# Kernel tuning notes

Measured on AMD Instinct MI355X. Metric: run time of the kernel, lower is better.

Reference implementation:

```python
import jax, jax.numpy as jnp
import numpy as np

COMMITMENT_COST = 0.25


def setup_inputs() -> dict:
    key = jax.random.key(0)
    k1, k2 = jax.random.split(key)
    cnt_emb = jax.random.normal(k1, (64, 2048, 80), dtype=jnp.float32)
    embed_weight = jax.random.normal(k2, (1024, 80), dtype=jnp.float32)  # nn.Embedding(n_embed, n_mel).weight
    return {"cnt_emb": cnt_emb, "embed_weight": embed_weight}


def reference(cnt_emb, embed_weight):
    # embed: detached, transposed [n_mel, n_embed], column-normalized (only for distance computation)
    embed = jax.lax.stop_gradient(embed_weight).T  # [80, 1024]
    embed = embed / jnp.linalg.norm(embed, axis=0, keepdims=True)

    flatten = jax.lax.stop_gradient(cnt_emb.reshape(-1, cnt_emb.shape[-1]))  # [N, 80]
    dist = (
        jnp.sum(flatten * flatten, axis=1, keepdims=True)
        - 2.0 * (flatten @ embed)
        + jnp.sum(embed * embed, axis=0, keepdims=True)
    )  # [N, n_embed]
    embed_ind = jnp.argmax(-dist, axis=1).reshape(cnt_emb.shape[:-1])  # [B, T]

    # gather from the UNnormalized embedding table (as nn.Embedding lookup)
    quantized = embed_weight[embed_ind]  # [B, T, 80]

    e_latent_loss = jnp.mean((jax.lax.stop_gradient(quantized) - cnt_emb) ** 2)
    q_latent_loss = jnp.mean((quantized - jax.lax.stop_gradient(cnt_emb)) ** 2)
    loss = q_latent_loss + COMMITMENT_COST * e_latent_loss

    # straight-through estimator
    quantized = cnt_emb + jax.lax.stop_gradient(quantized - cnt_emb)
    return quantized, loss
```

## Files before the change

kernel.cpp:

```cpp
#include <hip/hip_runtime.h>

#define D   80
#define NE  1024
#define CAP 32
#define MARGIN 0.5f

#define OFF_ACC  0
#define OFF_EN   64
#define OFF_EC   327744
#define OFF_ENBT 331840
#define OFF_BIDX 495680
#define OFF_CNT  1019968
#define OFF_LIST 1544256
#define WS_NEED  9932864

typedef __attribute__((ext_vector_type(8))) short  bf16x8;
typedef __attribute__((ext_vector_type(4))) float  f32x4;

static __device__ __forceinline__ short f2bf(float f) {
    unsigned u = __float_as_uint(f);
    return (short)((u + 0x7fffu + ((u >> 16) & 1u)) >> 16);
}

static __device__ __forceinline__ bf16x8 cvt8(const float* p) {
    float4 f0 = *(const float4*)p;
    float4 f1 = *(const float4*)(p + 4);
    bf16x8 a;
    a[0] = f2bf(f0.x); a[1] = f2bf(f0.y); a[2] = f2bf(f0.z); a[3] = f2bf(f0.w);
    a[4] = f2bf(f1.x); a[5] = f2bf(f1.y); a[6] = f2bf(f1.z); a[7] = f2bf(f1.w);
    return a;
}

static __device__ __forceinline__ void gload_lds16(const void* g, void* l) {
    __builtin_amdgcn_global_load_lds(
        (const __attribute__((address_space(1))) unsigned int*)g,
        (__attribute__((address_space(3))) unsigned int*)l, 16, 0, 0);
}

__global__ __launch_bounds__(256) void vq_prep(const float* __restrict__ w,
                                               float* __restrict__ en,
                                               float* __restrict__ ec,
                                               char* __restrict__ enbT) {
    int j = blockIdx.x * blockDim.x + threadIdx.x;
    if (j >= NE) return;
    const float* wj = w + j * D;
    float s = __fmul_rn(wj[0], wj[0]);
    for (int k = 1; k < D; ++k) s = __fadd_rn(s, __fmul_rn(wj[k], wj[k]));
    float norm = __fsqrt_rn(s);
    float* ej = en + j * D;
    float c = 0.f;
    for (int k = 0; k < D; ++k) {
        float v = __fdiv_rn(wj[k], norm);
        ej[k] = v;
        float sq = __fmul_rn(v, v);
        c = (k == 0) ? sq : __fadd_rn(c, sq);
    }
    ec[j] = c;
    for (int cc = 0; cc < 10; ++cc) {
        bf16x8 b;
#pragma unroll
        for (int e = 0; e < 8; ++e)
            b[e] = f2bf(__fmul_rn(-2.0f, ej[cc * 8 + e]));
        *(bf16x8*)(enbT + cc * 16384 + j * 16) = b;
    }
}

__global__ __launch_bounds__(256)
__attribute__((amdgpu_waves_per_eu(4, 4)))
void vq_mfma(
        const float* __restrict__ x,
        const char* __restrict__ enbT,
        int* __restrict__ cnt,
        unsigned short* __restrict__ list,
        int n) {
    __shared__ __align__(16) char lds[40960];

    const int tid  = threadIdx.x;
    const int lane = tid & 63;
    const int wv   = tid >> 6;
    const int row0 = blockIdx.x * 128 + wv * 32;
    const int l15  = lane & 15;
    const int lg   = lane >> 4;

    bf16x8 A0[2], A1[2], A2[2];
#pragma unroll
    for (int rt = 0; rt < 2; ++rt) {
        const float* xr = x + (size_t)(row0 + rt * 16 + l15) * D;
        A0[rt] = cvt8(xr + lg * 8);
        A1[rt] = cvt8(xr + 32 + lg * 8);
        if (lg < 2) A2[rt] = cvt8(xr + 64 + lg * 8);
        else { bf16x8 z = {}; A2[rt] = z; }
    }

    const int sl = wv * 1024 + lane * 16;

    float vmin[2][4];
#pragma unroll
    for (int rt = 0; rt < 2; ++rt)
#pragma unroll
        for (int r = 0; r < 4; ++r) vmin[rt][r] = 3.4e38f;

    for (int s = 0; s < 4; ++s) {
        __syncthreads();
#pragma unroll
        for (int c = 0; c < 10; ++c)
            gload_lds16(enbT + c * 16384 + s * 4096 + sl, lds + c * 4096 + sl);
        __syncthreads();

        for (int e16 = 0; e16 < 16; ++e16) {
            const char* base = lds + (e16 * 16 + l15) * 16;
            bf16x8 B0 = *(const bf16x8*)(base + lg * 4096);
            bf16x8 B1 = *(const bf16x8*)(base + (4 + lg) * 4096);
            bf16x8 B2 = *(const bf16x8*)(base + (8 + (lg & 1)) * 4096);
#pragma unroll
            for (int rt = 0; rt < 2; ++rt) {
                f32x4 c = {0.f, 0.f, 0.f, 0.f};
                c = __builtin_amdgcn_mfma_f32_16x16x32_bf16(A0[rt], B0, c, 0, 0, 0);
                c = __builtin_amdgcn_mfma_f32_16x16x32_bf16(A1[rt], B1, c, 0, 0, 0);
                c = __builtin_amdgcn_mfma_f32_16x16x32_bf16(A2[rt], B2, c, 0, 0, 0);
#pragma unroll
                for (int r = 0; r < 4; ++r) vmin[rt][r] = fminf(vmin[rt][r], c[r]);
            }
        }
    }

    float thr[2][4];
#pragma unroll
    for (int rt = 0; rt < 2; ++rt)
#pragma unroll
        for (int r = 0; r < 4; ++r) {
            float v = vmin[rt][r];
#pragma unroll
            for (int m = 1; m < 16; m <<= 1) v = fminf(v, __shfl_xor(v, m));
            thr[rt][r] = v + MARGIN;
        }

    for (int s = 0; s < 4; ++s) {
        __syncthreads();
#pragma unroll
        for (int c = 0; c < 10; ++c)
            gload_lds16(enbT + c * 16384 + s * 4096 + sl, lds + c * 4096 + sl);
        __syncthreads();

        for (int e16 = 0; e16 < 16; ++e16) {
            const char* base = lds + (e16 * 16 + l15) * 16;
            bf16x8 B0 = *(const bf16x8*)(base + lg * 4096);
            bf16x8 B1 = *(const bf16x8*)(base + (4 + lg) * 4096);
            bf16x8 B2 = *(const bf16x8*)(base + (8 + (lg & 1)) * 4096);
            int jj = s * 256 + e16 * 16 + l15;
#pragma unroll
            for (int rt = 0; rt < 2; ++rt) {
                f32x4 c = {0.f, 0.f, 0.f, 0.f};
                c = __builtin_amdgcn_mfma_f32_16x16x32_bf16(A0[rt], B0, c, 0, 0, 0);
                c = __builtin_amdgcn_mfma_f32_16x16x32_bf16(A1[rt], B1, c, 0, 0, 0);
                c = __builtin_amdgcn_mfma_f32_16x16x32_bf16(A2[rt], B2, c, 0, 0, 0);
                bool h0 = c[0] <= thr[rt][0], h1 = c[1] <= thr[rt][1];
                bool h2 = c[2] <= thr[rt][2], h3 = c[3] <= thr[rt][3];
                if (__any(h0 | h1 | h2 | h3)) {
#pragma unroll
                    for (int r = 0; r < 4; ++r) {
                        bool h = (r == 0) ? h0 : (r == 1) ? h1 : (r == 2) ? h2 : h3;
                        if (h) {
                            int row = row0 + rt * 16 + lg * 4 + r;
                            int o = atomicAdd(cnt + row, 1);
                            if (o < CAP)
                                list[(size_t)row * CAP + o] = (unsigned short)jj;
                        }
                    }
                }
            }
        }
    }
}

__global__ __launch_bounds__(256)
__attribute__((amdgpu_waves_per_eu(1, 2)))
void vq_exact(const float* __restrict__ x,
              const float* __restrict__ en,
              const float* __restrict__ ec,
              const int* __restrict__ cnt,
              const unsigned short* __restrict__ list,
              int* __restrict__ bidx, int n) {
    int row = blockIdx.x * 256 + threadIdx.x;
    if (row >= n) return;
    float X[D];
    const float4* x4 = (const float4*)(x + (size_t)row * D);
#pragma unroll
    for (int i = 0; i < D / 4; ++i) {
        float4 v = x4[i];
        X[4 * i + 0] = v.x; X[4 * i + 1] = v.y;
        X[4 * i + 2] = v.z; X[4 * i + 3] = v.w;
    }
    float pr[8];
#pragma unroll
    for (int t = 0; t < 8; ++t) pr[t] = __fmul_rn(X[t], X[t]);
#pragma unroll
    for (int base = 8; base < D; base += 8)
#pragma unroll
        for (int t = 0; t < 8; ++t)
            pr[t] = __fadd_rn(pr[t], __fmul_rn(X[base + t], X[base + t]));
    float A = __fadd_rn(
        __fadd_rn(__fadd_rn(pr[0], pr[1]), __fadd_rn(pr[2], pr[3])),
        __fadd_rn(__fadd_rn(pr[4], pr[5]), __fadd_rn(pr[6], pr[7])));

    float best = 3.4e38f;
    int bi = -1;
    int c = cnt[row];
    if (c > 0 && c <= CAP) {
        for (int i = 0; i < c; ++i) {
            int j = list[(size_t)row * CAP + i];
            const float* ej = en + j * D;
            float d = 0.f;
#pragma unroll
            for (int k = 0; k < D; ++k) d = __builtin_fmaf(X[k], ej[k], d);
            float s = __fadd_rn(__fsub_rn(A, __fmul_rn(2.0f, d)), ec[j]);
            if (s < best || (s == best && j < bi)) { best = s; bi = j; }
        }
    } else {
        for (int j = 0; j < NE; ++j) {
            const float* ej = en + j * D;
            float d = 0.f;
#pragma unroll
            for (int k = 0; k < D; ++k) d = __builtin_fmaf(X[k], ej[k], d);
            float s = __fadd_rn(__fsub_rn(A, __fmul_rn(2.0f, d)), ec[j]);
            if (s < best) { best = s; bi = j; }
        }
    }
    bidx[row] = bi;
}

__global__ __launch_bounds__(256) void vq_epi(
        const float* __restrict__ x,
        const float* __restrict__ w,
        const int* __restrict__ bidx,
        float* __restrict__ out,
        double* __restrict__ loss_acc, int n) {
    const int row0 = blockIdx.x * 64;
    double ss = 0.0;
    for (int f = threadIdx.x; f < 64 * (D / 4); f += 256) {
        int row = f / (D / 4);
        int gr  = row0 + row;
        if (gr < n) {
            int k4  = (f % (D / 4)) * 4;
            int gbi = bidx[gr];
            float4 q  = *(const float4*)(w + gbi * D + k4);
            float4 xv = *(const float4*)(x + (size_t)gr * D + k4);
            float d0 = __fsub_rn(q.x, xv.x), d1 = __fsub_rn(q.y, xv.y);
            float d2 = __fsub_rn(q.z, xv.z), d3 = __fsub_rn(q.w, xv.w);
            float4 o;
            o.x = __fadd_rn(xv.x, d0); o.y = __fadd_rn(xv.y, d1);
            o.z = __fadd_rn(xv.z, d2); o.w = __fadd_rn(xv.w, d3);
            *(float4*)(out + (size_t)gr * D + k4) = o;
            ss += (double)__fmul_rn(d0, d0) + (double)__fmul_rn(d1, d1);
            ss += (double)__fmul_rn(d2, d2) + (double)__fmul_rn(d3, d3);
        }
    }
#pragma unroll
    for (int off = 32; off > 0; off >>= 1) ss += __shfl_down(ss, off);
    __shared__ double bsum[4];
    int wid = threadIdx.x >> 6;
    if ((threadIdx.x & 63) == 0) bsum[wid] = ss;
    __syncthreads();
    if (threadIdx.x == 0)
        atomicAdd(loss_acc, bsum[0] + bsum[1] + bsum[2] + bsum[3]);
}

__global__ void vq_fin_kernel(const double* __restrict__ acc,
                              float* __restrict__ out_loss,
                              double count) {
    float m = (float)(*acc / count);
    *out_loss = __fadd_rn(m, __fmul_rn(0.25f, m));
}

__global__ __launch_bounds__(64)
__attribute__((amdgpu_waves_per_eu(2, 2)))
void vq_main_exact(const float* __restrict__ x, const float* __restrict__ w,
                   const float* __restrict__ en, const float* __restrict__ ec,
                   float* __restrict__ out, double* __restrict__ loss_acc, int n) {
    const int r = blockIdx.x * 64 + threadIdx.x;
    double ss = 0.0;
    if (r < n) {
        float X[D];
        const float4* x4 = (const float4*)(x + (size_t)r * D);
#pragma unroll
        for (int i = 0; i < D / 4; ++i) {
            float4 v = x4[i];
            X[4 * i + 0] = v.x; X[4 * i + 1] = v.y;
            X[4 * i + 2] = v.z; X[4 * i + 3] = v.w;
        }
        float pr[8];
#pragma unroll
        for (int t = 0; t < 8; ++t) pr[t] = __fmul_rn(X[t], X[t]);
#pragma unroll
        for (int base = 8; base < D; base += 8)
#pragma unroll
            for (int t = 0; t < 8; ++t)
                pr[t] = __fadd_rn(pr[t], __fmul_rn(X[base + t], X[base + t]));
        float A = __fadd_rn(
            __fadd_rn(__fadd_rn(pr[0], pr[1]), __fadd_rn(pr[2], pr[3])),
            __fadd_rn(__fadd_rn(pr[4], pr[5]), __fadd_rn(pr[6], pr[7])));
        float best = 3.4e38f; int bi = 0;
        for (int j = 0; j < NE; ++j) {
            const float* ej = en + j * D;
            float d = 0.f;
#pragma unroll
            for (int k = 0; k < D; ++k) d = __builtin_fmaf(X[k], ej[k], d);
            float s = __fadd_rn(__fsub_rn(A, __fmul_rn(2.0f, d)), ec[j]);
            if (s < best) { best = s; bi = j; }
        }
        const float* wj = w + bi * D;
        float4* o4 = (float4*)(out + (size_t)r * D);
#pragma unroll
        for (int i = 0; i < D / 4; ++i) {
            float q0 = wj[4*i+0], q1 = wj[4*i+1], q2 = wj[4*i+2], q3 = wj[4*i+3];
            float d0 = __fsub_rn(q0, X[4*i+0]), d1 = __fsub_rn(q1, X[4*i+1]);
            float d2 = __fsub_rn(q2, X[4*i+2]), d3 = __fsub_rn(q3, X[4*i+3]);
            float4 o;
            o.x = __fadd_rn(X[4*i+0], d0); o.y = __fadd_rn(X[4*i+1], d1);
            o.z = __fadd_rn(X[4*i+2], d2); o.w = __fadd_rn(X[4*i+3], d3);
            o4[i] = o;
            ss += (double)__fmul_rn(d0, d0) + (double)__fmul_rn(d1, d1);
            ss += (double)__fmul_rn(d2, d2) + (double)__fmul_rn(d3, d3);
        }
    }
#pragma unroll
    for (int off = 32; off > 0; off >>= 1) ss += __shfl_down(ss, off);
    if (threadIdx.x == 0) atomicAdd(loss_acc, ss);
}

extern "C" void kernel_launch(void* const* d_in, const int* in_sizes, int n_in,
                              void* d_out, int out_size, void* d_ws, size_t ws_size,
                              hipStream_t stream) {
    const float* x = (const float*)d_in[0];
    const float* w = (const float*)d_in[1];
    float* out = (float*)d_out;
    int n = in_sizes[0] / D;

    char* ws = (char*)d_ws;
    double* acc = (double*)(ws + OFF_ACC);
    float*  en  = (float*)(ws + OFF_EN);
    float*  ec  = (float*)(ws + OFF_EC);

    hipMemsetAsync(ws + OFF_ACC, 0, 64, stream);
    if (ws_size >= WS_NEED) {
        char*  enbT = ws + OFF_ENBT;
        int*   bidx = (int*)(ws + OFF_BIDX);
        int*   cnt  = (int*)(ws + OFF_CNT);
        unsigned short* list = (unsigned short*)(ws + OFF_LIST);
        hipMemsetAsync(cnt, 0, (size_t)n * 4, stream);
        vq_prep<<<(NE + 255) / 256, 256, 0, stream>>>(w, en, ec, enbT);
        vq_mfma<<<n / 128, 256, 0, stream>>>(x, enbT, cnt, list, n);
        vq_exact<<<(n + 255) / 256, 256, 0, stream>>>(x, en, ec, cnt, list, bidx, n);
        vq_epi<<<(n + 63) / 64, 256, 0, stream>>>(x, w, bidx, out, acc, n);
    } else {
        char* enbT_dummy = ws + OFF_EC + 4096;
        vq_prep<<<(NE + 255) / 256, 256, 0, stream>>>(w, en, ec, enbT_dummy);
        vq_main_exact<<<(n + 63) / 64, 64, 0, stream>>>(x, w, en, ec, out, acc, n);
    }
    vq_fin_kernel<<<1, 1, 0, stream>>>(acc, out + (size_t)n * D, (double)n * D);
}
```

Measured before the change: 177.6 us.

## Double-buffer codebook staging in MFMA pass and fuse exact rescoring with epilogue

The MFMA distance kernel now stages the bf16 codebook into two half-size LDS buffers in 128-entry chunks. The next chunk's global-to-LDS load is issued while the current one is consumed, which removes one barrier per step and overlaps load latency with MFMA work. Separately, the exact-rescoring kernel and the epilogue kernel are fused: best indices go through shared memory instead of a global bidx array, saving a launch and a global round trip. In exchange the epilogue now runs under the rescoring kernel's low-occupancy launch bounds, and the double-buffer scheme relies on a single barrier per iteration being enough to avoid overwriting a buffer that is still being read.

```diff
diff --git a/kernel.cpp b/kernel.cpp
--- a/kernel.cpp
+++ b/kernel.cpp
@@ -2,6 +2,8 @@
 
 #define D   80
 #define NE  1024
+#define HS  128
+#define NH  (NE / HS)
 #define CAP 32
 #define MARGIN 0.5f
 
@@ -9,7 +11,6 @@
 #define OFF_EN   64
 #define OFF_EC   327744
 #define OFF_ENBT 331840
-#define OFF_BIDX 495680
 #define OFF_CNT  1019968
 #define OFF_LIST 1544256
 #define WS_NEED  9932864
@@ -73,7 +74,7 @@
         int* __restrict__ cnt,
         unsigned short* __restrict__ list,
         int n) {
-    __shared__ __align__(16) char lds[40960];
+    __shared__ __align__(16) char lds[2][20480];
 
     const int tid  = threadIdx.x;
     const int lane = tid & 63;
@@ -92,7 +93,15 @@
         else { bf16x8 z = {}; A2[rt] = z; }
     }
 
-    const int sl = wv * 1024 + lane * 16;
+#define STAGE(b, h) do {                                                      \
+        _Pragma("unroll")                                                     \
+        for (int t = 0; t < 5; ++t) {                                         \
+            int slot = tid + t * 256;                                         \
+            gload_lds16(enbT + (size_t)(slot >> 7) * 16384 + (h) * 2048       \
+                             + (slot & 127) * 16,                             \
+                        &lds[b][0] + slot * 16);                              \
+        }                                                                     \
+    } while (0)
 
     float vmin[2][4];
 #pragma unroll
@@ -100,18 +109,16 @@
 #pragma unroll
         for (int r = 0; r < 4; ++r) vmin[rt][r] = 3.4e38f;
 
-    for (int s = 0; s < 4; ++s) {
+    STAGE(0, 0);
+    for (int h = 0; h < NH; ++h) {
         __syncthreads();
-#pragma unroll
-        for (int c = 0; c < 10; ++c)
-            gload_lds16(enbT + c * 16384 + s * 4096 + sl, lds + c * 4096 + sl);
-        __syncthreads();
-
-        for (int e16 = 0; e16 < 16; ++e16) {
-            const char* base = lds + (e16 * 16 + l15) * 16;
-            bf16x8 B0 = *(const bf16x8*)(base + lg * 4096);
-            bf16x8 B1 = *(const bf16x8*)(base + (4 + lg) * 4096);
-            bf16x8 B2 = *(const bf16x8*)(base + (8 + (lg & 1)) * 4096);
+        if (h + 1 < NH) STAGE((h + 1) & 1, h + 1);
+        const char* buf = &lds[h & 1][0];
+        for (int e16 = 0; e16 < 8; ++e16) {
+            const char* base = buf + (e16 * 16 + l15) * 16;
+            bf16x8 B0 = *(const bf16x8*)(base + lg * 2048);
+            bf16x8 B1 = *(const bf16x8*)(base + (4 + lg) * 2048);
+            bf16x8 B2 = *(const bf16x8*)(base + (8 + (lg & 1)) * 2048);
 #pragma unroll
             for (int rt = 0; rt < 2; ++rt) {
                 f32x4 c = {0.f, 0.f, 0.f, 0.f};
@@ -135,19 +142,17 @@
             thr[rt][r] = v + MARGIN;
         }
 
-    for (int s = 0; s < 4; ++s) {
+    STAGE(0, 0);
+    for (int h = 0; h < NH; ++h) {
         __syncthreads();
-#pragma unroll
-        for (int c = 0; c < 10; ++c)
-            gload_lds16(enbT + c * 16384 + s * 4096 + sl, lds + c * 4096 + sl);
-        __syncthreads();
-
-        for (int e16 = 0; e16 < 16; ++e16) {
-            const char* base = lds + (e16 * 16 + l15) * 16;
-            bf16x8 B0 = *(const bf16x8*)(base + lg * 4096);
-            bf16x8 B1 = *(const bf16x8*)(base + (4 + lg) * 4096);
-            bf16x8 B2 = *(const bf16x8*)(base + (8 + (lg & 1)) * 4096);
-            int jj = s * 256 + e16 * 16 + l15;
+        if (h + 1 < NH) STAGE((h + 1) & 1, h + 1);
+        const char* buf = &lds[h & 1][0];
+        for (int e16 = 0; e16 < 8; ++e16) {
+            const char* base = buf + (e16 * 16 + l15) * 16;
+            bf16x8 B0 = *(const bf16x8*)(base + lg * 2048);
+            bf16x8 B1 = *(const bf16x8*)(base + (4 + lg) * 2048);
+            bf16x8 B2 = *(const bf16x8*)(base + (8 + (lg & 1)) * 2048);
+            int jj = h * HS + e16 * 16 + l15;
 #pragma unroll
             for (int rt = 0; rt < 2; ++rt) {
                 f32x4 c = {0.f, 0.f, 0.f, 0.f};
@@ -159,8 +164,8 @@
                 if (__any(h0 | h1 | h2 | h3)) {
 #pragma unroll
                     for (int r = 0; r < 4; ++r) {
-                        bool h = (r == 0) ? h0 : (r == 1) ? h1 : (r == 2) ? h2 : h3;
-                        if (h) {
+                        bool hh = (r == 0) ? h0 : (r == 1) ? h1 : (r == 2) ? h2 : h3;
+                        if (hh) {
                             int row = row0 + rt * 16 + lg * 4 + r;
                             int o = atomicAdd(cnt + row, 1);
                             if (o < CAP)
@@ -171,78 +176,82 @@
             }
         }
     }
+#undef STAGE
 }
 
 __global__ __launch_bounds__(256)
 __attribute__((amdgpu_waves_per_eu(1, 2)))
-void vq_exact(const float* __restrict__ x,
-              const float* __restrict__ en,
-              const float* __restrict__ ec,
-              const int* __restrict__ cnt,
-              const unsigned short* __restrict__ list,
-              int* __restrict__ bidx, int n) {
-    int row = blockIdx.x * 256 + threadIdx.x;
-    if (row >= n) return;
-    float X[D];
-    const float4* x4 = (const float4*)(x + (size_t)row * D);
-#pragma unroll
-    for (int i = 0; i < D / 4; ++i) {
-        float4 v = x4[i];
-        X[4 * i + 0] = v.x; X[4 * i + 1] = v.y;
-        X[4 * i + 2] = v.z; X[4 * i + 3] = v.w;
-    }
-    float pr[8];
-#pragma unroll
-    for (int t = 0; t < 8; ++t) pr[t] = __fmul_rn(X[t], X[t]);
-#pragma unroll
-    for (int base = 8; base < D; base += 8)
-#pragma unroll
-        for (int t = 0; t < 8; ++t)
-            pr[t] = __fadd_rn(pr[t], __fmul_rn(X[base + t], X[base + t]));
-    float A = __fadd_rn(
-        __fadd_rn(__fadd_rn(pr[0], pr[1]), __fadd_rn(pr[2], pr[3])),
-        __fadd_rn(__fadd_rn(pr[4], pr[5]), __fadd_rn(pr[6], pr[7])));
-
-    float best = 3.4e38f;
-    int bi = -1;
-    int c = cnt[row];
-    if (c > 0 && c <= CAP) {
-        for (int i = 0; i < c; ++i) {
-            int j = list[(size_t)row * CAP + i];
-            const float* ej = en + j * D;
-            float d = 0.f;
-#pragma unroll
-            for (int k = 0; k < D; ++k) d = __builtin_fmaf(X[k], ej[k], d);
-            float s = __fadd_rn(__fsub_rn(A, __fmul_rn(2.0f, d)), ec[j]);
-            if (s < best || (s == best && j < bi)) { best = s; bi = j; }
-        }
-    } else {
-        for (int j = 0; j < NE; ++j) {
-            const float* ej = en + j * D;
-            float d = 0.f;
-#pragma unroll
-            for (int k = 0; k < D; ++k) d = __builtin_fmaf(X[k], ej[k], d);
-            float s = __fadd_rn(__fsub_rn(A, __fmul_rn(2.0f, d)), ec[j]);
-            if (s < best) { best = s; bi = j; }
-        }
-    }
-    bidx[row] = bi;
-}
-
-__global__ __launch_bounds__(256) void vq_epi(
-        const float* __restrict__ x,
-        const float* __restrict__ w,
-        const int* __restrict__ bidx,
-        float* __restrict__ out,
-        double* __restrict__ loss_acc, int n) {
-    const int row0 = blockIdx.x * 64;
+void vq_exact_epi(const float* __restrict__ x,
+                  const float* __restrict__ en,
+                  const float* __restrict__ ec,
+                  const int* __restrict__ cnt,
+                  const unsigned short* __restrict__ list,
+                  const float* __restrict__ w,
+                  float* __restrict__ out,
+                  double* __restrict__ loss_acc, int n) {
+    __shared__ int sbidx[256];
+    __shared__ double bsum[4];
+    const int row = blockIdx.x * 256 + threadIdx.x;
+
+    int bi = 0;
+    if (row < n) {
+        float X[D];
+        const float4* x4 = (const float4*)(x + (size_t)row * D);
+#pragma unroll
+        for (int i = 0; i < D / 4; ++i) {
+            float4 v = x4[i];
+            X[4 * i + 0] = v.x; X[4 * i + 1] = v.y;
+            X[4 * i + 2] = v.z; X[4 * i + 3] = v.w;
+        }
+        float pr[8];
+#pragma unroll
+        for (int t = 0; t < 8; ++t) pr[t] = __fmul_rn(X[t], X[t]);
+#pragma unroll
+        for (int base = 8; base < D; base += 8)
+#pragma unroll
+            for (int t = 0; t < 8; ++t)
+                pr[t] = __fadd_rn(pr[t], __fmul_rn(X[base + t], X[base + t]));
+        float A = __fadd_rn(
+            __fadd_rn(__fadd_rn(pr[0], pr[1]), __fadd_rn(pr[2], pr[3])),
+            __fadd_rn(__fadd_rn(pr[4], pr[5]), __fadd_rn(pr[6], pr[7])));
+
+        float best = 3.4e38f;
+        bi = -1;
+        int c = cnt[row];
+        if (c > 0 && c <= CAP) {
+            for (int i = 0; i < c; ++i) {
+                int j = list[(size_t)row * CAP + i];
+                const float* ej = en + j * D;
+                float d = 0.f;
+#pragma unroll
+                for (int k = 0; k < D; ++k) d = __builtin_fmaf(X[k], ej[k], d);
+                float s = __fadd_rn(__fsub_rn(A, __fmul_rn(2.0f, d)), ec[j]);
+                if (s < best || (s == best && j < bi)) { best = s; bi = j; }
+            }
+        } else {
+            for (int j = 0; j < NE; ++j) {
+                const float* ej = en + j * D;
+                float d = 0.f;
+#pragma unroll
+                for (int k = 0; k < D; ++k) d = __builtin_fmaf(X[k], ej[k], d);
+                float s = __fadd_rn(__fsub_rn(A, __fmul_rn(2.0f, d)), ec[j]);
+                if (s < best) { best = s; bi = j; }
+            }
+        }
+    }
+    sbidx[threadIdx.x] = bi;
+    __syncthreads();
+
+    const int row0 = blockIdx.x * 256;
     double ss = 0.0;
-    for (int f = threadIdx.x; f < 64 * (D / 4); f += 256) {
-        int row = f / (D / 4);
-        int gr  = row0 + row;
+#pragma unroll
+    for (int t = 0; t < 20; ++t) {
+        int f  = threadIdx.x + t * 256;
+        int rr = f / 20;
+        int k4 = (f % 20) * 4;
+        int gr = row0 + rr;
         if (gr < n) {
-            int k4  = (f % (D / 4)) * 4;
-            int gbi = bidx[gr];
+            int gbi = sbidx[rr];
             float4 q  = *(const float4*)(w + gbi * D + k4);
             float4 xv = *(const float4*)(x + (size_t)gr * D + k4);
             float d0 = __fsub_rn(q.x, xv.x), d1 = __fsub_rn(q.y, xv.y);
@@ -257,7 +266,6 @@
     }
 #pragma unroll
     for (int off = 32; off > 0; off >>= 1) ss += __shfl_down(ss, off);
-    __shared__ double bsum[4];
     int wid = threadIdx.x >> 6;
     if ((threadIdx.x & 63) == 0) bsum[wid] = ss;
     __syncthreads();
@@ -344,14 +352,13 @@
     hipMemsetAsync(ws + OFF_ACC, 0, 64, stream);
     if (ws_size >= WS_NEED) {
         char*  enbT = ws + OFF_ENBT;
-        int*   bidx = (int*)(ws + OFF_BIDX);
         int*   cnt  = (int*)(ws + OFF_CNT);
         unsigned short* list = (unsigned short*)(ws + OFF_LIST);
         hipMemsetAsync(cnt, 0, (size_t)n * 4, stream);
         vq_prep<<<(NE + 255) / 256, 256, 0, stream>>>(w, en, ec, enbT);
         vq_mfma<<<n / 128, 256, 0, stream>>>(x, enbT, cnt, list, n);
-        vq_exact<<<(n + 255) / 256, 256, 0, stream>>>(x, en, ec, cnt, list, bidx, n);
-        vq_epi<<<(n + 63) / 64, 256, 0, stream>>>(x, w, bidx, out, acc, n);
+        vq_exact_epi<<<(n + 255) / 256, 256, 0, stream>>>(x, en, ec, cnt, list,
+                                                          w, out, acc, n);
     } else {
         char* enbT_dummy = ws + OFF_EC + 4096;
         vq_prep<<<(NE + 255) / 256, 256, 0, stream>>>(w, en, ec, enbT_dummy);
```

Result: faster. 156.1 us (-12.1%).
